# Optimization experiments

Hardware: AMD Instinct MI355X
Metric: run time of the kernel (lower is better)

## Reference

```python
import jax, jax.numpy as jnp
import numpy as np


def _sq_cdist(a, b):
    # squared Euclidean distances, [N, M]
    a2 = jnp.sum(a * a, axis=1)[:, None]
    b2 = jnp.sum(b * b, axis=1)[None, :]
    d = a2 + b2 - 2.0 * (a @ b.T)
    return jnp.maximum(d, 0.0)


def _gaussian_kernel_mean(a, b, sigmas):
    # mean over N*M of sum_k exp(-dist / (2*sigma_k))
    dist = _sq_cdist(a, b)                      # [N, M]
    beta = 1.0 / (2.0 * sigmas)                 # [K]
    s = jnp.exp(-beta[:, None, None] * dist[None, :, :])  # [K, N, M]
    return jnp.mean(jnp.sum(s, axis=0))


def setup_inputs() -> dict:
    key = jax.random.key(0)
    k1, k2 = jax.random.split(key)
    B, C, H, W = 4, 256, 32, 32
    x = jax.random.normal(k1, (B, C, H, W), dtype=jnp.float32)
    y = jax.random.normal(k2, (B, C, H, W), dtype=jnp.float32)
    sigmas = jnp.array([0.01, 0.1, 1.0, 10.0, 100.0], dtype=jnp.float32)
    return {"x": x, "y": y, "sigmas": sigmas}


def reference(x, y, sigmas):
    B, C, H, W = x.shape
    # (B,C,H,W) -> (B*H*W, C), matching flatten(2).transpose(1,2).reshape(-1,C)
    xf = jnp.transpose(x.reshape(B, C, H * W), (0, 2, 1)).reshape(-1, C)
    yf = jnp.transpose(y.reshape(B, C, H * W), (0, 2, 1)).reshape(-1, C)
    xx = _gaussian_kernel_mean(xf, xf, sigmas)
    yy = _gaussian_kernel_mean(yf, yf, sigmas)
    xy = _gaussian_kernel_mean(xf, yf, sigmas)
    return xx + yy - 2.0 * xy
```

## Files before the change

kernel.cpp:

```cpp
#include <hip/hip_runtime.h>
#include <hip/hip_bf16.h>


#define NSIG 5
#define CKS   262144
#define NBLK2 2080
#define GRIDP 694

typedef __attribute__((ext_vector_type(8))) short short8;
typedef __attribute__((ext_vector_type(4))) float floatx4;

__global__ __launch_bounds__(256) void prep_kernel(const float* __restrict__ x,
                                                   const float* __restrict__ y,
                                                   ushort* __restrict__ Zc,
                                                   float* __restrict__ norms) {
    const int bid = blockIdx.x;
    const int t = threadIdx.x;
    const int s = bid >> 8;
    const int b = (bid >> 6) & 3;
    const int p0 = (bid & 63) << 4;
    const float* src = s ? y : x;
    const int n0 = (s << 12) + (b << 10) + p0;

    __shared__ float tile[256][17];

    const int cg = t >> 2;
    const int p4 = (t & 3) << 2;
#pragma unroll
    for (int pass = 0; pass < 4; ++pass) {
        const int c = cg + (pass << 6);
        const float4 v = *(const float4*)(src + (((size_t)((b << 8) + c)) << 10) + p0 + p4);
        tile[c][p4] = v.x; tile[c][p4 + 1] = v.y; tile[c][p4 + 2] = v.z; tile[c][p4 + 3] = v.w;
    }
    __syncthreads();

    const int r = t >> 4;
    const int q = t & 15;
    const int row = n0 + r;
    const int sw = (row >> 1) & 3;
    float nsum = 0.f;
#pragma unroll
    for (int h = 0; h < 2; ++h) {
        const int j = q + (h << 4);
        const int ck = j >> 2;
        const int sq = (j & 3) ^ sw;
        const int c0 = j << 3;
        uint pk[4];
#pragma unroll
        for (int jj = 0; jj < 4; ++jj) {
            const float f0 = tile[c0 + 2 * jj][r];
            const float f1 = tile[c0 + 2 * jj + 1][r];
            const __hip_bfloat16 h0 = __float2bfloat16(f0);
            const __hip_bfloat16 h1 = __float2bfloat16(f1);
            const float q0 = __bfloat162float(h0), q1 = __bfloat162float(h1);
            nsum = fmaf(q0, q0, nsum);
            nsum = fmaf(q1, q1, nsum);
            pk[jj] = (uint)(*(const ushort*)&h0) | ((uint)(*(const ushort*)&h1) << 16);
        }
        *(uint4*)(Zc + (size_t)ck * CKS + (size_t)row * 32 + (sq << 3)) =
            make_uint4(pk[0], pk[1], pk[2], pk[3]);
    }
#pragma unroll
    for (int off = 1; off < 16; off <<= 1) nsum += __shfl_xor(nsum, off, 32);
    if (q == 0) norms[row] = nsum;
}

__device__ __forceinline__ void decode_tile(int lin, int w, int& i0, int& j0,
                                            bool& active, bool& diag) {
    int p = (int)((-4.0f + sqrtf(16.0f + 128.0f * (float)lin)) * (1.0f / 64.0f));
    p = p < 0 ? 0 : (p > 7 ? 7 : p);
    while (p < 7 && 32 * (p + 1) * (p + 1) + 4 * (p + 1) <= lin) ++p;
    while (p > 0 && 32 * p * p + 4 * p > lin) --p;
    const int o = lin - (32 * p * p + 4 * p);
    int c = 7;
#pragma unroll
    for (int cc = 7; cc >= 1; --cc) {
        const int Q = cc * (8 * p + 1) + (cc * (cc - 1)) / 2;
        if (o < Q) c = cc - 1;
    }
    const int Qc = c * (8 * p + 1) + (c * (c - 1)) / 2;
    const int tj2 = 8 * p + c;
    const int ti2 = o - Qc;
    const int ti = (ti2 << 1) + (w >> 1);
    const int tj = (tj2 << 1) + (w & 1);
    active = (ti <= tj);
    diag = (ti == tj);
    i0 = ti << 6;
    j0 = tj << 6;
}

__device__ __forceinline__ void tile_offsets(int i0, int j0, int m, int q,
                                             int* offA, int* offB) {
#pragma unroll
    for (int f = 0; f < 4; ++f) {
        const int ra = i0 + (f << 4) + m;
        offA[f] = (ra << 5) + ((q ^ ((ra >> 1) & 3)) << 3);
        const int rb = j0 + (f << 4) + m;
        offB[f] = (rb << 5) + ((q ^ ((rb >> 1) & 3)) << 3);
    }
}

__global__ __launch_bounds__(256, 3) void gemm_epi(const ushort* __restrict__ Zc,
                                                   const float* __restrict__ norms,
                                                   const float* __restrict__ sigmas,
                                                   float* __restrict__ partials) {
    __shared__ float wsum[4];

    const int t = threadIdx.x;
    const int w = t >> 6, l = t & 63;
    const int m = l & 15, q = l >> 4;

    float c2[NSIG];
#pragma unroll
    for (int k = 0; k < NSIG; ++k) c2[k] = (-0.5f / sigmas[k]) * 1.44269504f;

    int lin = blockIdx.x;
    int i0, j0;
    bool active, diag;
    decode_tile(lin, w, i0, j0, active, diag);
    int offA[4], offB[4];
    tile_offsets(i0, j0, m, q, offA, offB);

    short8 curA[4], curB[4];
#pragma unroll
    for (int f = 0; f < 4; ++f) {
        curA[f] = *(const short8*)(Zc + offA[f]);
        curB[f] = *(const short8*)(Zc + offB[f]);
    }

    float lsum = 0.f;

#pragma unroll 1
    for (;;) {
        floatx4 accf[4][4];
#pragma unroll
        for (int fi = 0; fi < 4; ++fi)
#pragma unroll
            for (int fj = 0; fj < 4; ++fj) accf[fi][fj] = (floatx4){0.f, 0.f, 0.f, 0.f};

        short8 nxtA[4], nxtB[4];
#pragma unroll
        for (int ck = 0; ck < 8; ++ck) {
            if (ck < 7) {
                const size_t ko = (size_t)(ck + 1) * CKS;
#pragma unroll
                for (int f = 0; f < 4; ++f) {
                    nxtA[f] = *(const short8*)(Zc + ko + offA[f]);
                    nxtB[f] = *(const short8*)(Zc + ko + offB[f]);
                }
            }
#pragma unroll
            for (int fi = 0; fi < 4; ++fi)
#pragma unroll
                for (int fj = 0; fj < 4; ++fj)
                    accf[fi][fj] = __builtin_amdgcn_mfma_f32_16x16x32_bf16(curA[fi], curB[fj], accf[fi][fj], 0, 0, 0);
            if (ck < 7) {
#pragma unroll
                for (int f = 0; f < 4; ++f) { curA[f] = nxtA[f]; curB[f] = nxtB[f]; }
            }
        }

        const int ei0 = i0, ej0 = j0;
        const bool eact = active, ediag = diag;
        const float esgn2 = ((ei0 < 4096) == (ej0 < 4096)) ? 2.f : -2.f;

        floatx4 ni4[4];
        float njs[4];
#pragma unroll
        for (int fi = 0; fi < 4; ++fi)
            ni4[fi] = *(const floatx4*)(norms + ei0 + (fi << 4) + (q << 2));
#pragma unroll
        for (int fj = 0; fj < 4; ++fj)
            njs[fj] = norms[ej0 + (fj << 4) + m];

        const int lin2 = lin + GRIDP;
        const bool have2 = (lin2 < NBLK2);
        if (have2) {
            decode_tile(lin2, w, i0, j0, active, diag);
            tile_offsets(i0, j0, m, q, offA, offB);
#pragma unroll
            for (int f = 0; f < 4; ++f) {
                curA[f] = *(const short8*)(Zc + offA[f]);
                curB[f] = *(const short8*)(Zc + offB[f]);
            }
        }

        if (eact) {
#pragma unroll
            for (int fi = 0; fi < 4; ++fi) {
#pragma unroll
                for (int fj = 0; fj < 4; ++fj) {
#pragma unroll
                    for (int v = 0; v < 4; ++v) {
                        float d = fmaf(-2.f, accf[fi][fj][v], ni4[fi][v] + njs[fj]);
                        d = fmaxf(d, 0.f);
                        if (ediag) {
                            const int dif = ((fi - fj) << 4) + ((q << 2) + v) - m;
                            d = (dif < 0) ? d : 3.0e9f;
                        }
                        accf[fi][fj][v] = d;
                    }
                }
            }

            float dmin = accf[0][0][0];
#pragma unroll
            for (int fi = 0; fi < 4; ++fi)
#pragma unroll
                for (int fj = 0; fj < 4; ++fj)
#pragma unroll
                    for (int v = 0; v < 4; ++v) dmin = fminf(dmin, accf[fi][fj][v]);
#pragma unroll
            for (int off = 1; off < 64; off <<= 1) dmin = fminf(dmin, __shfl_xor(dmin, off, 64));

            float tsum = 0.f;
#pragma unroll
            for (int k = 0; k < NSIG; ++k) {
                if (c2[k] * dmin >= -126.f) {
#pragma unroll
                    for (int fi = 0; fi < 4; ++fi)
#pragma unroll
                        for (int fj = 0; fj < 4; ++fj)
#pragma unroll
                            for (int v = 0; v < 4; ++v)
                                tsum += __builtin_amdgcn_exp2f(c2[k] * accf[fi][fj][v]);
                }
            }
            lsum = fmaf(esgn2, tsum, lsum);
        }

        lin = lin2;
        if (!have2) break;
    }

#pragma unroll
    for (int off = 32; off > 0; off >>= 1) lsum += __shfl_down(lsum, off, 64);
    if (l == 0) wsum[w] = lsum;
    __syncthreads();
    if (t == 0) partials[blockIdx.x] = wsum[0] + wsum[1] + wsum[2] + wsum[3];
}

__global__ __launch_bounds__(256) void finalize_kernel(const float* __restrict__ partials,
                                                       float* __restrict__ out) {
    __shared__ double sh[256];
    const int t = threadIdx.x;
    double s = 0.0;
    for (int i = t; i < GRIDP; i += 256) s += (double)partials[i];
    sh[t] = s;
    __syncthreads();
    for (int st = 128; st > 0; st >>= 1) {
        if (t < st) sh[t] += sh[t + st];
        __syncthreads();
    }
    if (t == 0) out[0] = (float)((sh[0] + 8192.0 * NSIG) * (1.0 / (4096.0 * 4096.0)));
}

extern "C" void kernel_launch(void* const* d_in, const int* in_sizes, int n_in,
                              void* d_out, int out_size, void* d_ws, size_t ws_size,
                              hipStream_t stream) {
    const float* x   = (const float*)d_in[0];
    const float* y   = (const float*)d_in[1];
    const float* sig = (const float*)d_in[2];

    ushort* Zc      = (ushort*)d_ws;
    float* norms    = (float*)((char*)d_ws + (size_t)8192 * 256 * 2);
    float* partials = (float*)((char*)norms + 8192 * sizeof(float));
    float* out      = (float*)d_out;

    prep_kernel<<<512, 256, 0, stream>>>(x, y, Zc, norms);
    gemm_epi<<<GRIDP, 256, 0, stream>>>(Zc, norms, sig, partials);
    finalize_kernel<<<1, 256, 0, stream>>>(partials, out);
}
```

Measured before the change: 96.67 us.

## Deepen register prefetch to two K-chunks and lower occupancy to 2 waves

Replaces the single-stage global-to-register prefetch in the bf16 MFMA GEMM loop with a two-stage pipeline, loading chunk ck+2 while computing chunk ck. The next tile's first two chunks are also preloaded during the epilogue. The aim is to hide more global-load latency behind MFMA work. In exchange it uses more VGPRs, so launch bounds drop from 3 to 2 blocks per CU, which lowers occupancy.

```diff
diff --git a/kernel.cpp b/kernel.cpp
--- a/kernel.cpp
+++ b/kernel.cpp
@@ -100,7 +100,7 @@
     }
 }
 
-__global__ __launch_bounds__(256, 3) void gemm_epi(const ushort* __restrict__ Zc,
+__global__ __launch_bounds__(256, 2) void gemm_epi(const ushort* __restrict__ Zc,
                                                    const float* __restrict__ norms,
                                                    const float* __restrict__ sigmas,
                                                    float* __restrict__ partials) {
@@ -121,11 +121,16 @@
     int offA[4], offB[4];
     tile_offsets(i0, j0, m, q, offA, offB);
 
-    short8 curA[4], curB[4];
+    short8 A0[4], B0[4], A1[4], B1[4];
 #pragma unroll
     for (int f = 0; f < 4; ++f) {
-        curA[f] = *(const short8*)(Zc + offA[f]);
-        curB[f] = *(const short8*)(Zc + offB[f]);
+        A0[f] = *(const short8*)(Zc + offA[f]);
+        B0[f] = *(const short8*)(Zc + offB[f]);
+    }
+#pragma unroll
+    for (int f = 0; f < 4; ++f) {
+        A1[f] = *(const short8*)(Zc + CKS + offA[f]);
+        B1[f] = *(const short8*)(Zc + CKS + offB[f]);
     }
 
     float lsum = 0.f;
@@ -138,25 +143,29 @@
 #pragma unroll
             for (int fj = 0; fj < 4; ++fj) accf[fi][fj] = (floatx4){0.f, 0.f, 0.f, 0.f};
 
-        short8 nxtA[4], nxtB[4];
 #pragma unroll
         for (int ck = 0; ck < 8; ++ck) {
+            short8 ldA[4], ldB[4];
+            if (ck < 6) {
+                const size_t ko = (size_t)(ck + 2) * CKS;
+#pragma unroll
+                for (int f = 0; f < 4; ++f) {
+                    ldA[f] = *(const short8*)(Zc + ko + offA[f]);
+                    ldB[f] = *(const short8*)(Zc + ko + offB[f]);
+                }
+            }
+#pragma unroll
+            for (int fi = 0; fi < 4; ++fi)
+#pragma unroll
+                for (int fj = 0; fj < 4; ++fj)
+                    accf[fi][fj] = __builtin_amdgcn_mfma_f32_16x16x32_bf16(A0[fi], B0[fj], accf[fi][fj], 0, 0, 0);
             if (ck < 7) {
-                const size_t ko = (size_t)(ck + 1) * CKS;
-#pragma unroll
-                for (int f = 0; f < 4; ++f) {
-                    nxtA[f] = *(const short8*)(Zc + ko + offA[f]);
-                    nxtB[f] = *(const short8*)(Zc + ko + offB[f]);
-                }
-            }
-#pragma unroll
-            for (int fi = 0; fi < 4; ++fi)
-#pragma unroll
-                for (int fj = 0; fj < 4; ++fj)
-                    accf[fi][fj] = __builtin_amdgcn_mfma_f32_16x16x32_bf16(curA[fi], curB[fj], accf[fi][fj], 0, 0, 0);
-            if (ck < 7) {
-#pragma unroll
-                for (int f = 0; f < 4; ++f) { curA[f] = nxtA[f]; curB[f] = nxtB[f]; }
+#pragma unroll
+                for (int f = 0; f < 4; ++f) { A0[f] = A1[f]; B0[f] = B1[f]; }
+            }
+            if (ck < 6) {
+#pragma unroll
+                for (int f = 0; f < 4; ++f) { A1[f] = ldA[f]; B1[f] = ldB[f]; }
             }
         }
 
@@ -180,8 +189,13 @@
             tile_offsets(i0, j0, m, q, offA, offB);
 #pragma unroll
             for (int f = 0; f < 4; ++f) {
-                curA[f] = *(const short8*)(Zc + offA[f]);
-                curB[f] = *(const short8*)(Zc + offB[f]);
+                A0[f] = *(const short8*)(Zc + offA[f]);
+                B0[f] = *(const short8*)(Zc + offB[f]);
+            }
+#pragma unroll
+            for (int f = 0; f < 4; ++f) {
+                A1[f] = *(const short8*)(Zc + CKS + offA[f]);
+                B1[f] = *(const short8*)(Zc + CKS + offB[f]);
             }
         }
 
```

Measured after the change: 99.45 us. 1.03x slower.
